# Kernel optimization log

Measured on AMD Instinct MI355X. Metric: run time of the kernel, lower is better.

Reference implementation:

```python
import jax, jax.numpy as jnp
import numpy as np

QMAX = 7.0      # symmetric int4 magnitude
GROUP = 64      # weight quant group size along input dim
RANK = 32       # SVD low-rank correction rank
EPS = 1e-8


def quantize_act(x):
    # per-token symmetric int4 fake-quant: scale = max|x| / 7 over feature dim
    s = jnp.maximum(jnp.max(jnp.abs(x), axis=-1, keepdims=True) / QMAX, EPS)
    q = jnp.clip(jnp.round(x / s), -8.0, 7.0)
    return q * s


def quantize_weight(w):
    # per-output-channel, per-group (GROUP along input dim) symmetric int4 fake-quant
    O, D = w.shape
    wg = w.reshape(O, D // GROUP, GROUP)
    s = jnp.maximum(jnp.max(jnp.abs(wg), axis=-1, keepdims=True) / QMAX, EPS)
    q = jnp.clip(jnp.round(wg / s), -8.0, 7.0)
    return (q * s).reshape(O, D)


def setup_inputs() -> dict:
    key = jax.random.key(0)
    k0, k1, k2, k3 = jax.random.split(key, 4)
    dim_in, dim_out2 = 3072, 24576
    x = jax.random.normal(k0, (1, 4096, dim_in), dtype=jnp.float32)
    w_res = jax.random.normal(k1, (dim_out2, dim_in), dtype=jnp.float32) * 0.02
    lora_down = jax.random.normal(k2, (RANK, dim_in), dtype=jnp.float32) * 0.02
    lora_up = jax.random.normal(k3, (dim_out2, RANK), dtype=jnp.float32) * 0.02
    return {"x": x, "w_res": w_res, "lora_down": lora_down, "lora_up": lora_up}


def reference(x, w_res, lora_down, lora_up):
    # SVDQW4A4Linear: quantized residual matmul + fp low-rank correction
    xq = quantize_act(x)                        # [B, S, D]
    wq = quantize_weight(w_res)                 # [O, D]
    out = jnp.einsum('bsd,od->bso', xq, wq)
    out = out + jnp.einsum('bsr,or->bso', jnp.einsum('bsd,rd->bsr', x, lora_down), lora_up)
    # GEGLU epilogue: chunk(2, dim=-1), x * gelu(gate)  (torch F.gelu = exact erf)
    h, gate = jnp.split(out, 2, axis=-1)
    return h * jax.nn.gelu(gate, approximate=False)
```

## Files before the change

kernel.cpp:

```cpp
#include <hip/hip_runtime.h>
#include <hip/hip_bf16.h>
#include <math.h>

typedef __bf16 bf16_t;
typedef __bf16 bf16x4 __attribute__((ext_vector_type(4)));
typedef __bf16 bf16x8 __attribute__((ext_vector_type(8)));
typedef float  f32x4  __attribute__((ext_vector_type(4)));

#define DIN   3072
#define NOUT  24576
#define HALF  12288
#define MTOK  4096
#define BM    128
#define BN    128
#define BK    64

#define NB_LORA  (MTOK / 8)
#define NB_QX    (MTOK)
#define NB_CVT   (NOUT * 32 / 4 / 256)
#define NB_QW    (NOUT * (DIN / 4) / 256)
#define B0       (NB_LORA)
#define B1       (B0 + NB_QX)
#define B2       (B1 + NB_CVT)
#define NB_PREP  (B2 + NB_QW)

#define GLD16(gp, lp) \
    __builtin_amdgcn_global_load_lds((const __attribute__((address_space(1))) void*)(gp), \
                                     (__attribute__((address_space(3))) void*)(lp), 16, 0, 0)

__global__ __launch_bounds__(256) void k_prep(const float* __restrict__ x,
                                              const float* __restrict__ w,
                                              const float* __restrict__ ld,
                                              const float* __restrict__ lu,
                                              bf16_t* __restrict__ xq,
                                              bf16_t* __restrict__ wq,
                                              bf16_t* __restrict__ T,
                                              bf16_t* __restrict__ lub) {
    const int bid = blockIdx.x;
    const int t = threadIdx.x;

    if (bid < B0) {
        int r = t & 31;
        int m = bid * 8 + (t >> 5);
        const float4* xr = reinterpret_cast<const float4*>(x + (size_t)m * DIN);
        const float4* lr = reinterpret_cast<const float4*>(ld + (size_t)r * DIN);
        float acc = 0.f;
#pragma unroll 4
        for (int i = 0; i < DIN / 4; ++i) {
            float4 a = xr[i], b = lr[i];
            acc += a.x * b.x + a.y * b.y + a.z * b.z + a.w * b.w;
        }
        T[(size_t)m * 32 + r] = (bf16_t)acc;
    } else if (bid < B1) {
        int m = bid - B0;
        const float4* row = reinterpret_cast<const float4*>(x + (size_t)m * DIN);
        float4 v[3];
        float vm = 0.f;
#pragma unroll
        for (int i = 0; i < 3; ++i) {
            v[i] = row[t + i * 256];
            vm = fmaxf(vm, fmaxf(fmaxf(fabsf(v[i].x), fabsf(v[i].y)),
                                 fmaxf(fabsf(v[i].z), fabsf(v[i].w))));
        }
#pragma unroll
        for (int d = 1; d < 64; d <<= 1) vm = fmaxf(vm, __shfl_xor(vm, d));
        __shared__ float sm[4];
        if ((t & 63) == 0) sm[t >> 6] = vm;
        __syncthreads();
        vm = fmaxf(fmaxf(sm[0], sm[1]), fmaxf(sm[2], sm[3]));
        float s = fmaxf(vm * (1.f / 7.f), 1e-8f);
        float inv = 1.f / s;
        bf16x4* orow = reinterpret_cast<bf16x4*>(xq + (size_t)m * DIN);
#pragma unroll
        for (int i = 0; i < 3; ++i) {
            bf16x4 o;
            o[0] = (bf16_t)(fminf(fmaxf(rintf(v[i].x * inv), -8.f), 7.f) * s);
            o[1] = (bf16_t)(fminf(fmaxf(rintf(v[i].y * inv), -8.f), 7.f) * s);
            o[2] = (bf16_t)(fminf(fmaxf(rintf(v[i].z * inv), -8.f), 7.f) * s);
            o[3] = (bf16_t)(fminf(fmaxf(rintf(v[i].w * inv), -8.f), 7.f) * s);
            orow[t + i * 256] = o;
        }
    } else if (bid < B2) {
        size_t idx = (size_t)(bid - B1) * 256 + t;
        float4 v = reinterpret_cast<const float4*>(lu)[idx];
        bf16x4 o;
        o[0] = (bf16_t)v.x; o[1] = (bf16_t)v.y; o[2] = (bf16_t)v.z; o[3] = (bf16_t)v.w;
        reinterpret_cast<bf16x4*>(lub)[idx] = o;
    } else {
        size_t idx = (size_t)(bid - B2) * 256 + t;
        float4 v = reinterpret_cast<const float4*>(w)[idx];
        float vm = fmaxf(fmaxf(fabsf(v.x), fabsf(v.y)), fmaxf(fabsf(v.z), fabsf(v.w)));
        vm = fmaxf(vm, __shfl_xor(vm, 1));
        vm = fmaxf(vm, __shfl_xor(vm, 2));
        vm = fmaxf(vm, __shfl_xor(vm, 4));
        vm = fmaxf(vm, __shfl_xor(vm, 8));
        float s = fmaxf(vm * (1.f / 7.f), 1e-8f);
        float inv = 1.f / s;
        bf16x4 o;
        o[0] = (bf16_t)(fminf(fmaxf(rintf(v.x * inv), -8.f), 7.f) * s);
        o[1] = (bf16_t)(fminf(fmaxf(rintf(v.y * inv), -8.f), 7.f) * s);
        o[2] = (bf16_t)(fminf(fmaxf(rintf(v.z * inv), -8.f), 7.f) * s);
        o[3] = (bf16_t)(fminf(fmaxf(rintf(v.w * inv), -8.f), 7.f) * s);
        reinterpret_cast<bf16x4*>(wq)[idx] = o;
    }
}

__global__ __launch_bounds__(512, 2) void k_gemm(const bf16_t* __restrict__ xq,
                                                 const bf16_t* __restrict__ wq,
                                                 const bf16_t* __restrict__ T,
                                                 const bf16_t* __restrict__ lub,
                                                 float* __restrict__ out) {
    __shared__ __align__(16) char smem[65536];
    bf16_t* sA = (bf16_t*)smem;
    bf16_t* sH = sA + BM * BK;
    bf16_t* sG = sH + BN * BK;

    int tid = threadIdx.x, lane = tid & 63, w = tid >> 6;
    int half = w >> 2;
    int wr = (w & 3) >> 1, wc = w & 1;

    int nwg = gridDim.x;
    int cpx = nwg >> 3;
    int swz = (blockIdx.x & 7) * cpx + (blockIdx.x >> 3);
    int mt = swz & 31, nt = swz >> 5;
    int m0 = mt * BM, c0 = nt * BN;

    f32x4 acc[4][4];
#pragma unroll
    for (int i = 0; i < 4; ++i)
#pragma unroll
        for (int j = 0; j < 4; ++j) acc[i][j] = (f32x4){0.f, 0.f, 0.f, 0.f};

    const char* sBb = (const char*)(half ? sG : sH);
    const char* sAb = (const char*)sA;

    for (int k0 = 0; k0 < DIN; k0 += BK) {
        __syncthreads();
#pragma unroll
        for (int r = 0; r < 2; ++r) {
            int chunk = r * 512 + tid;
            int row = chunk >> 3;
            int gc = ((chunk & 7) ^ (row & 7)) * 8;
            int ldsoff = r * 4096 + w * 512;
            GLD16(xq + (size_t)(m0 + row) * DIN + k0 + gc, sA + ldsoff);
            GLD16(wq + (size_t)(c0 + row) * DIN + k0 + gc, sH + ldsoff);
            GLD16(wq + (size_t)(c0 + HALF + row) * DIN + k0 + gc, sG + ldsoff);
        }
        __syncthreads();

#pragma unroll
        for (int ks = 0; ks < 2; ++ks) {
            int c16 = ks * 4 + (lane >> 4);
            bf16x8 a[4], b[4];
#pragma unroll
            for (int i = 0; i < 4; ++i) {
                int ra = wr * 64 + i * 16 + (lane & 15);
                int rb = wc * 64 + i * 16 + (lane & 15);
                a[i] = *reinterpret_cast<const bf16x8*>(sAb + ra * 128 + ((c16 ^ (ra & 7)) << 4));
                b[i] = *reinterpret_cast<const bf16x8*>(sBb + rb * 128 + ((c16 ^ (rb & 7)) << 4));
            }
#pragma unroll
            for (int m = 0; m < 4; ++m)
#pragma unroll
                for (int n = 0; n < 4; ++n)
                    acc[m][n] = __builtin_amdgcn_mfma_f32_16x16x32_bf16(a[m], b[n], acc[m][n], 0, 0, 0);
        }
    }

    {
        bf16x8 tf[4];
#pragma unroll
        for (int m = 0; m < 4; ++m)
            tf[m] = *reinterpret_cast<const bf16x8*>(
                T + (size_t)(m0 + wr * 64 + m * 16 + (lane & 15)) * 32 + (lane >> 4) * 8);
#pragma unroll
        for (int n = 0; n < 4; ++n) {
            bf16x8 lu = *reinterpret_cast<const bf16x8*>(
                lub + (size_t)(c0 + half * HALF + wc * 64 + n * 16 + (lane & 15)) * 32 + (lane >> 4) * 8);
#pragma unroll
            for (int m = 0; m < 4; ++m)
                acc[m][n] = __builtin_amdgcn_mfma_f32_16x16x32_bf16(tf[m], lu, acc[m][n], 0, 0, 0);
        }
    }

    __syncthreads();
    float* exch = (float*)smem;
    if (half) {
#pragma unroll
        for (int m = 0; m < 4; ++m)
#pragma unroll
            for (int n = 0; n < 4; ++n) {
                int col = wc * 64 + n * 16 + (lane & 15);
#pragma unroll
                for (int r = 0; r < 4; ++r) {
                    int row = wr * 64 + m * 16 + (lane >> 4) * 4 + r;
                    float g = acc[m][n][r];
                    float gl = 0.5f * g * (1.0f + erff(g * 0.70710678118654752f));
                    exch[row * 128 + (col ^ (((row >> 2) & 3) << 4))] = gl;
                }
            }
    }
    __syncthreads();
    if (!half) {
#pragma unroll
        for (int m = 0; m < 4; ++m)
#pragma unroll
            for (int n = 0; n < 4; ++n) {
                int col = wc * 64 + n * 16 + (lane & 15);
#pragma unroll
                for (int r = 0; r < 4; ++r) {
                    int row = wr * 64 + m * 16 + (lane >> 4) * 4 + r;
                    float gl = exch[row * 128 + (col ^ (((row >> 2) & 3) << 4))];
                    out[(size_t)(m0 + row) * HALF + c0 + col] = acc[m][n][r] * gl;
                }
            }
    }
}

extern "C" void kernel_launch(void* const* d_in, const int* in_sizes, int n_in,
                              void* d_out, int out_size, void* d_ws, size_t ws_size,
                              hipStream_t stream) {
    const float* x  = (const float*)d_in[0];
    const float* wr = (const float*)d_in[1];
    const float* ld = (const float*)d_in[2];
    const float* lu = (const float*)d_in[3];
    float* out = (float*)d_out;

    bf16_t* xq  = (bf16_t*)d_ws;
    bf16_t* wq  = xq + (size_t)MTOK * DIN;
    bf16_t* T   = wq + (size_t)NOUT * DIN;
    bf16_t* lub = T  + (size_t)MTOK * 32;

    k_prep<<<NB_PREP, 256, 0, stream>>>(x, wr, ld, lu, xq, wq, T, lub);
    k_gemm<<<(MTOK / BM) * (HALF / BN), 512, 0, stream>>>(xq, wq, T, lub, out);
}
```

Measured before the change: 848.4 us.

## Triple-buffer GEMM LDS tiles with async global_load_lds prefetch pipeline

Replaces the load-sync-compute loop in the GEMM with a three-stage LDS ring buffer. Three K-tiles are prefetched up front, and each iteration waits only for the oldest tile via `s_waitcnt vmcnt(12)` and a raw barrier before issuing the next tile's loads. Global pointers are precomputed per thread and advanced incrementally, which removes the per-iteration address math. The aim is to hide global memory latency behind MFMA work. In exchange, LDS use rises to 144KB, which likely cuts residency from two workgroups to one per CU, and near the end of K some redundant reloads of the last tile are issued.

```diff
diff --git a/kernel.cpp b/kernel.cpp
--- a/kernel.cpp
+++ b/kernel.cpp
@@ -14,6 +14,7 @@
 #define BM    128
 #define BN    128
 #define BK    64
+#define NT    48
 
 #define NB_LORA  (MTOK / 8)
 #define NB_QX    (MTOK)
@@ -27,6 +28,10 @@
 #define GLD16(gp, lp) \
     __builtin_amdgcn_global_load_lds((const __attribute__((address_space(1))) void*)(gp), \
                                      (__attribute__((address_space(3))) void*)(lp), 16, 0, 0)
+
+#define BAR()    __builtin_amdgcn_s_barrier()
+#define WAITV(N) asm volatile("s_waitcnt vmcnt(" #N ")" ::: "memory")
+#define SCHED0() __builtin_amdgcn_sched_barrier(0)
 
 __global__ __launch_bounds__(256) void k_prep(const float* __restrict__ x,
                                               const float* __restrict__ w,
@@ -105,15 +110,19 @@
     }
 }
 
+#define STAGE3(buf)                                                           \
+    do {                                                                      \
+        GLD16(pAl, (buf) + wq1);            GLD16(pAh, (buf) + wq1 + 8192);   \
+        GLD16(pHl, (buf) + 16384 + wq1);    GLD16(pHh, (buf) + 24576 + wq1);  \
+        GLD16(pGl, (buf) + 32768 + wq1);    GLD16(pGh, (buf) + 40960 + wq1);  \
+    } while (0)
+
 __global__ __launch_bounds__(512, 2) void k_gemm(const bf16_t* __restrict__ xq,
                                                  const bf16_t* __restrict__ wq,
                                                  const bf16_t* __restrict__ T,
                                                  const bf16_t* __restrict__ lub,
                                                  float* __restrict__ out) {
-    __shared__ __align__(16) char smem[65536];
-    bf16_t* sA = (bf16_t*)smem;
-    bf16_t* sH = sA + BM * BK;
-    bf16_t* sG = sH + BN * BK;
+    __shared__ __align__(16) char smem[147456];
 
     int tid = threadIdx.x, lane = tid & 63, w = tid >> 6;
     int half = w >> 2;
@@ -131,22 +140,31 @@
 #pragma unroll
         for (int j = 0; j < 4; ++j) acc[i][j] = (f32x4){0.f, 0.f, 0.f, 0.f};
 
-    const char* sBb = (const char*)(half ? sG : sH);
-    const char* sAb = (const char*)sA;
-
-    for (int k0 = 0; k0 < DIN; k0 += BK) {
-        __syncthreads();
-#pragma unroll
-        for (int r = 0; r < 2; ++r) {
-            int chunk = r * 512 + tid;
-            int row = chunk >> 3;
-            int gc = ((chunk & 7) ^ (row & 7)) * 8;
-            int ldsoff = r * 4096 + w * 512;
-            GLD16(xq + (size_t)(m0 + row) * DIN + k0 + gc, sA + ldsoff);
-            GLD16(wq + (size_t)(c0 + row) * DIN + k0 + gc, sH + ldsoff);
-            GLD16(wq + (size_t)(c0 + HALF + row) * DIN + k0 + gc, sG + ldsoff);
-        }
-        __syncthreads();
+    const int srow = tid >> 3;
+    const int sgc = ((tid & 7) ^ (srow & 7)) * 8;
+    const int wq1 = tid * 16;
+    const bf16_t* pAl = xq + (size_t)(m0 + srow) * DIN + sgc;
+    const bf16_t* pAh = pAl + (size_t)64 * DIN;
+    const bf16_t* pHl = wq + (size_t)(c0 + srow) * DIN + sgc;
+    const bf16_t* pHh = pHl + (size_t)64 * DIN;
+    const bf16_t* pGl = pHl + (size_t)HALF * DIN;
+    const bf16_t* pGh = pGl + (size_t)64 * DIN;
+
+#pragma unroll
+    for (int p = 0; p < 3; ++p) {
+        char* buf = smem + p * 49152;
+        STAGE3(buf);
+        pAl += BK; pAh += BK; pHl += BK; pHh += BK; pGl += BK; pGh += BK;
+    }
+
+    int cb = 0;
+    for (int t = 0; t < NT; ++t) {
+        WAITV(12);
+        BAR();
+        SCHED0();
+
+        const char* sAb = smem + cb * 49152;
+        const char* sBb = sAb + 16384 + (half << 14);
 
 #pragma unroll
         for (int ks = 0; ks < 2; ++ks) {
@@ -165,6 +183,18 @@
                 for (int n = 0; n < 4; ++n)
                     acc[m][n] = __builtin_amdgcn_mfma_f32_16x16x32_bf16(a[m], b[n], acc[m][n], 0, 0, 0);
         }
+
+        BAR();
+        SCHED0();
+
+        {
+            char* buf = smem + cb * 49152;
+            STAGE3(buf);
+        }
+        const int adv = (t + 4 < NT) ? BK : 0;
+        pAl += adv; pAh += adv; pHl += adv; pHh += adv; pGl += adv; pGh += adv;
+
+        cb = (cb == 2) ? 0 : cb + 1;
     }
 
     {
@@ -183,6 +213,7 @@
         }
     }
 
+    WAITV(0);
     __syncthreads();
     float* exch = (float*)smem;
     if (half) {
```

Measured after the change: 955.1 us. +12.6%, slower.
